# Kernel tuning notes

Measured on AMD Instinct MI355X. Metric: run time of the kernel, lower is better.

The kernel has to match this reference:

```python
import jax, jax.numpy as jnp
import numpy as np

B, S, C, OUT = 8, 2048, 1024, 1024

def setup_inputs() -> dict:
    key = jax.random.key(0)
    ks = jax.random.split(key, 10)
    s = C ** -0.5
    return {
        "input": jax.random.normal(ks[0], (B, S, C), jnp.float32),
        "memory": jax.random.normal(ks[1], (B, S, C), jnp.float32),
        "Wq": jax.random.normal(ks[2], (C, C), jnp.float32) * s,
        "bq": jnp.zeros((C,), jnp.float32),
        "Wk": jax.random.normal(ks[3], (C, C), jnp.float32) * s,
        "bk": jnp.zeros((C,), jnp.float32),
        "Wv": jax.random.normal(ks[4], (C, C), jnp.float32) * s,
        "bv": jnp.zeros((C,), jnp.float32),
        "Wo": jax.random.normal(ks[5], (OUT, C), jnp.float32) * s,
        "bo": jnp.zeros((OUT,), jnp.float32),
    }

def reference(input, memory, Wq, bq, Wk, bk, Wv, bv, Wo, bo):
    depth_scale = input.shape[2] ** -0.5
    q = (input @ Wq.T + bq) * depth_scale          # [B, Sq, C]
    k = memory @ Wk.T + bk                          # [B, Sk, C]
    v = memory @ Wv.T + bv                          # [B, Sk, C]
    logit = jnp.einsum('bqc,bkc->bqk', q, k)        # [B, Sq, Sk]
    attn = jax.nn.softmax(logit, axis=-1)
    sel = jnp.einsum('bqk,bkc->bqc', attn, v)       # [B, Sq, C]
    return sel @ Wo.T + bo                          # [B, Sq, OUT]
```

## Files before the change

### kernel.cpp

```cpp
#include <hip/hip_runtime.h>
#include <hip/hip_bf16.h>


typedef __attribute__((ext_vector_type(8))) short short8;
typedef __attribute__((ext_vector_type(4))) float f32x4;

static __device__ __forceinline__ unsigned short f2bf(float f) {
  union { float f; unsigned u; } x; x.f = f;
  unsigned r = x.u + 0x7FFFu + ((x.u >> 16) & 1u);
  return (unsigned short)(r >> 16);
}

static __device__ __forceinline__ long long brickoff(int r_, int k_, int Kd) {
  return (long long)(r_ >> 7) * ((long long)128 * Kd) +
         (long long)(k_ >> 5) * 4096 +
         (r_ & 127) * 32 +
         (((((k_ >> 3) & 3) ^ ((r_ >> 1) & 3))) << 3) +
         (k_ & 7);
}

__global__ __launch_bounds__(256) void cvt_brick_kernel(
    const float* __restrict__ s0, const float* __restrict__ s1,
    unsigned short* __restrict__ o0, unsigned short* __restrict__ o1,
    long long ngran) {
  const float* src = blockIdx.y ? s1 : s0;
  unsigned short* dst = blockIdx.y ? o1 : o0;
  long long gid = (long long)blockIdx.x * 256 + threadIdx.x;
  const long long stride = (long long)gridDim.x * 256;
  for (; gid < ngran; gid += stride) {
    const int tile = (int)(gid >> 14);
    const int g2 = (int)(gid & 16383);
    const int ks = g2 >> 9;
    const int rp = g2 & 511;
    const int r = rp >> 2;
    const int p = rp & 3;
    const int g = p ^ ((r >> 1) & 3);
    const float* sp = src + (long long)(tile * 128 + r) * 1024 + ks * 32 + g * 8;
    float4 u0 = ((const float4*)sp)[0];
    float4 u1 = ((const float4*)sp)[1];
    short8 pk;
    pk[0] = (short)f2bf(u0.x); pk[1] = (short)f2bf(u0.y);
    pk[2] = (short)f2bf(u0.z); pk[3] = (short)f2bf(u0.w);
    pk[4] = (short)f2bf(u1.x); pk[5] = (short)f2bf(u1.y);
    pk[6] = (short)f2bf(u1.z); pk[7] = (short)f2bf(u1.w);
    *(short8*)&dst[gid * 8] = pk;
  }
}

__global__ __launch_bounds__(256) void wcvt_brick_kernel(
    const float* __restrict__ w0, const float* __restrict__ w1,
    const float* __restrict__ w2, const float* __restrict__ w3,
    unsigned short* __restrict__ o0, unsigned short* __restrict__ o1,
    unsigned short* __restrict__ o2, unsigned short* __restrict__ o3) {
  const float* src; unsigned short* dst;
  switch (blockIdx.y) {
    case 0: src = w0; dst = o0; break;
    case 1: src = w1; dst = o1; break;
    case 2: src = w2; dst = o2; break;
    default: src = w3; dst = o3; break;
  }
  const int gid = blockIdx.x * 256 + threadIdx.x;
  const int tile = gid >> 14;
  const int g2 = gid & 16383;
  const int ks = g2 >> 9;
  const int rp = g2 & 511;
  const int r = rp >> 2;
  const int p = rp & 3;
  const int g = p ^ ((r >> 1) & 3);
  const float* sp = src + (long long)(tile * 128 + r) * 1024 + ks * 32 + g * 8;
  float4 u0 = ((const float4*)sp)[0];
  float4 u1 = ((const float4*)sp)[1];
  short8 pk;
  pk[0] = (short)f2bf(u0.x); pk[1] = (short)f2bf(u0.y);
  pk[2] = (short)f2bf(u0.z); pk[3] = (short)f2bf(u0.w);
  pk[4] = (short)f2bf(u1.x); pk[5] = (short)f2bf(u1.y);
  pk[6] = (short)f2bf(u1.z); pk[7] = (short)f2bf(u1.w);
  *(short8*)&dst[(long long)gid * 8] = pk;
}

#define EPI_BF16 0
#define EPI_BF16_TRANS 1
#define EPI_EXP 2
#define EPI_PV 3
#define EPI_F32 4

template <int EPI, bool HAS_BIAS>
__global__ __launch_bounds__(256, 3) void gemm_kernel(
    const unsigned short* __restrict__ A, const unsigned short* __restrict__ B,
    const float* __restrict__ bias, void* __restrict__ Dv,
    int NT, int ldaK, int ldbK, int ldd,
    long long sA, long long sBflat, int sBslice, int kOffB,
    long long sD, float scale) {
  int i = blockIdx.x + gridDim.x * (blockIdx.y + gridDim.y * blockIdx.z);
  const int nwg = gridDim.x * gridDim.y * gridDim.z;
  int v = (i & 7) * (nwg >> 3) + (i >> 3);
  const int by = v % gridDim.y;
  int u = v / gridDim.y;
  const int bx = u % gridDim.x;
  const int bz = u / gridDim.x;

  const int bm = bx * 128;
  const int bn = by * 128;
  const int tid = threadIdx.x;
  const int lane = tid & 63;
  const int wid = tid >> 6;
  const int wr = (wid >> 1) * 64;
  const int wc = (wid & 1) * 64;
  const int fr = lane & 15;
  const int hi = lane >> 4;
  const int laneoff = fr * 32 + ((hi ^ ((fr >> 1) & 3)) << 3);

  f32x4 acc[4][4];
#pragma unroll
  for (int m = 0; m < 4; ++m)
#pragma unroll
    for (int n = 0; n < 4; ++n) acc[m][n] = (f32x4){0.f, 0.f, 0.f, 0.f};

  f32x4 asum[4];
  short8 ones;
#pragma unroll
  for (int m = 0; m < 4; ++m) asum[m] = (f32x4){0.f, 0.f, 0.f, 0.f};
#pragma unroll
  for (int j = 0; j < 8; ++j) ones[j] = (short)0x3F80;

  const unsigned short* Ap = A + bz * sA + (long long)(bm >> 7) * 128 * ldaK +
                             wr * 32 + laneoff;
  const unsigned short* Bp = B + bz * sBflat + (long long)(bn >> 7) * 128 * ldbK +
                             (long long)(kOffB + bz * sBslice) * 4096 +
                             wc * 32 + laneoff;

  short8 a0[4], b0[4], a1[4], b1[4];
  auto LDA = [&](short8 (&d)[4], int t) {
    const unsigned short* p = Ap + (long long)t * 4096;
#pragma unroll
    for (int m = 0; m < 4; ++m) d[m] = *(const short8*)(p + m * 512);
  };
  auto LDB = [&](short8 (&d)[4], int t) {
    const unsigned short* p = Bp + (long long)t * 4096;
#pragma unroll
    for (int n = 0; n < 4; ++n) d[n] = *(const short8*)(p + n * 512);
  };
  auto FMA = [&](short8 (&a)[4], short8 (&b)[4]) {
#pragma unroll
    for (int m = 0; m < 4; ++m)
#pragma unroll
      for (int n = 0; n < 4; ++n)
        acc[m][n] = __builtin_amdgcn_mfma_f32_16x16x32_bf16(a[m], b[n],
                                                            acc[m][n], 0, 0, 0);
    if (EPI == EPI_PV) {
#pragma unroll
      for (int m = 0; m < 4; ++m)
        asum[m] = __builtin_amdgcn_mfma_f32_16x16x32_bf16(a[m], ones,
                                                          asum[m], 0, 0, 0);
    }
  };

  LDA(a0, 0); LDB(b0, 0);
  LDA(a1, 1); LDB(b1, 1);
  for (int t = 0; t < NT - 2; t += 2) {
    FMA(a0, b0);
    LDA(a0, t + 2); LDB(b0, t + 2);
    FMA(a1, b1);
    LDA(a1, t + 3); LDB(b1, t + 3);
  }
  FMA(a0, b0);
  FMA(a1, b1);

  const int cr = hi * 4;
  const int cc = fr;
#pragma unroll
  for (int m = 0; m < 4; ++m) {
    const int row0 = bm + wr + m * 16 + cr;
#pragma unroll
    for (int n = 0; n < 4; ++n) {
      const int col = bn + wc + n * 16 + cc;
      const float bv = HAS_BIAS ? bias[col] : 0.f;
      if (EPI == EPI_F32) {
        float* D = (float*)Dv + bz * sD;
#pragma unroll
        for (int j = 0; j < 4; ++j)
          D[(long long)(row0 + j) * ldd + col] = acc[m][n][j] + bv;
      } else if (EPI == EPI_BF16) {
        unsigned short* D = (unsigned short*)Dv + bz * sD;
#pragma unroll
        for (int j = 0; j < 4; ++j)
          D[brickoff(row0 + j, col, ldd)] = f2bf((acc[m][n][j] + bv) * scale);
      } else if (EPI == EPI_BF16_TRANS) {
        unsigned short* D = (unsigned short*)Dv + bz * sD;
#pragma unroll
        for (int j = 0; j < 4; ++j)
          D[brickoff(col, row0 + j, ldd)] = f2bf((acc[m][n][j] + bv) * scale);
      } else if (EPI == EPI_EXP) {
        unsigned short* D = (unsigned short*)Dv + bz * sD;
#pragma unroll
        for (int j = 0; j < 4; ++j)
          D[brickoff(row0 + j, col, ldd)] = f2bf(__expf(acc[m][n][j]));
      } else {
        unsigned short* D = (unsigned short*)Dv + bz * sD;
#pragma unroll
        for (int j = 0; j < 4; ++j) {
          const float li = 1.f / asum[m][j];
          D[brickoff(row0 + j, col, ldd)] = f2bf(acc[m][n][j] * li);
        }
      }
    }
  }
}

extern "C" void kernel_launch(void* const* d_in, const int* in_sizes, int n_in,
                              void* d_out, int out_size, void* d_ws, size_t ws_size,
                              hipStream_t stream) {
  (void)in_sizes; (void)n_in; (void)out_size;
  const float* input  = (const float*)d_in[0];
  const float* memory = (const float*)d_in[1];
  const float* Wq = (const float*)d_in[2];
  const float* bq = (const float*)d_in[3];
  const float* Wk = (const float*)d_in[4];
  const float* bk = (const float*)d_in[5];
  const float* Wv = (const float*)d_in[6];
  const float* bv = (const float*)d_in[7];
  const float* Wo = (const float*)d_in[8];
  const float* bo = (const float*)d_in[9];
  float* out = (float*)d_out;

  const int S = 2048, C = 1024;
  const int CB = 4;
  const long long BS = 16384;
  const long long N_IN = BS * C;
  const long long N_W  = (long long)C * C;

  char* p = (char*)d_ws;
  auto alloc = [&](size_t bytes) {
    char* r = p;
    p += (bytes + 255) & ~(size_t)255;
    return r;
  };
  unsigned short* wqb  = (unsigned short*)alloc(N_W * 2);
  unsigned short* wkb  = (unsigned short*)alloc(N_W * 2);
  unsigned short* wvb  = (unsigned short*)alloc(N_W * 2);
  unsigned short* wob  = (unsigned short*)alloc(N_W * 2);
  unsigned short* Qb   = (unsigned short*)alloc(N_IN * 2);
  unsigned short* Kb   = (unsigned short*)alloc(N_IN * 2);
  unsigned short* Xb   = (unsigned short*)alloc(N_IN * 2);
  if ((size_t)(p - (char*)d_ws) > ws_size) return;

  unsigned short* Vt  = (unsigned short*)d_out;
  unsigned short* inb = (unsigned short*)d_out + N_IN;
  unsigned short* memb = Xb;
  unsigned short* Pt   = Xb;

  wcvt_brick_kernel<<<dim3(512, 4, 1), 256, 0, stream>>>(Wq, Wk, Wv, Wo,
                                                         wqb, wkb, wvb, wob);
  cvt_brick_kernel<<<dim3(2048, 2, 1), 256, 0, stream>>>(memory, input, memb, inb,
                                                         N_IN / 8);

  const float depth_scale = 0.03125f;

  gemm_kernel<EPI_BF16, true><<<dim3(128, 8, 1), 256, 0, stream>>>(
      memb, wkb, bk, Kb, 32, C, C, C, 0, 0, 0, 0, 0, 1.0f);
  gemm_kernel<EPI_BF16_TRANS, true><<<dim3(128, 8, 1), 256, 0, stream>>>(
      memb, wvb, bv, Vt, 32, C, C, (int)BS, 0, 0, 0, 0, 0, 1.0f);
  gemm_kernel<EPI_BF16, true><<<dim3(128, 8, 1), 256, 0, stream>>>(
      inb, wqb, bq, Qb, 32, C, C, C, 0, 0, 0, 0, 0, depth_scale);

  for (int c = 0; c < 8 / CB; ++c) {
    const long long qoff = (long long)c * CB * S * C;
    gemm_kernel<EPI_EXP, false><<<dim3(16, 16, CB), 256, 0, stream>>>(
        Qb + qoff, Kb + qoff, nullptr, Pt,
        32, C, C, S, (long long)S * C, (long long)S * C, 0, 0,
        (long long)S * S, 1.0f);
    gemm_kernel<EPI_PV, false><<<dim3(16, 8, CB), 256, 0, stream>>>(
        Pt, Vt, nullptr, Qb + qoff,
        64, S, (int)BS, C, (long long)S * S, 0, 64, c * CB * 64,
        (long long)S * C, 1.0f);
  }

  gemm_kernel<EPI_F32, true><<<dim3(128, 8, 1), 256, 0, stream>>>(
      Qb, wob, bo, out, 32, C, C, C, 0, 0, 0, 0, 0, 1.0f);
}
```

Measured before the change: 396.0 us.

## Template GEMM tile shape to 128x256 and restructure activation bf16 conversion

The GEMM kernel becomes templated on per-wave fragment counts, so most GEMMs use a 128x256 block tile (4x8 fragments per wave), with occupancy lowered to 2 waves per SIMD for the larger tiles. This halves the grid in N and raises operand reuse per loaded A fragment, cutting global/L2 load traffic per MFMA. The activation conversion kernel now has each thread read a contiguous 32-float row segment and write four swizzled 8-element granules, instead of one granule per thread in a grid-stride loop. In exchange, the larger tiles raise register pressure and leave fewer workgroups to fill the CUs.

```diff
diff --git a/kernel.cpp b/kernel.cpp
--- a/kernel.cpp
+++ b/kernel.cpp
@@ -21,29 +21,30 @@
 
 __global__ __launch_bounds__(256) void cvt_brick_kernel(
     const float* __restrict__ s0, const float* __restrict__ s1,
-    unsigned short* __restrict__ o0, unsigned short* __restrict__ o1,
-    long long ngran) {
+    unsigned short* __restrict__ o0, unsigned short* __restrict__ o1) {
   const float* src = blockIdx.y ? s1 : s0;
   unsigned short* dst = blockIdx.y ? o1 : o0;
-  long long gid = (long long)blockIdx.x * 256 + threadIdx.x;
-  const long long stride = (long long)gridDim.x * 256;
-  for (; gid < ngran; gid += stride) {
-    const int tile = (int)(gid >> 14);
-    const int g2 = (int)(gid & 16383);
-    const int ks = g2 >> 9;
-    const int rp = g2 & 511;
-    const int r = rp >> 2;
-    const int p = rp & 3;
-    const int g = p ^ ((r >> 1) & 3);
-    const float* sp = src + (long long)(tile * 128 + r) * 1024 + ks * 32 + g * 8;
-    float4 u0 = ((const float4*)sp)[0];
-    float4 u1 = ((const float4*)sp)[1];
+  const int gid = blockIdx.x * 256 + threadIdx.x;
+  const int wv = gid >> 6;
+  const int lane = gid & 63;
+  const int tile = wv >> 6;
+  const int r = (wv & 63) * 2 + (lane & 1);
+  const int ks = lane >> 1;
+  const float* sp = src + (long long)(tile * 128 + r) * 1024 + ks * 32;
+  float4 u[8];
+#pragma unroll
+  for (int i = 0; i < 8; ++i) u[i] = ((const float4*)sp)[i];
+  const int x = (r >> 1) & 3;
+  unsigned short* dp = dst + (long long)tile * 131072 + ks * 4096 + r * 32;
+#pragma unroll
+  for (int p = 0; p < 4; ++p) {
+    const int g = p ^ x;
     short8 pk;
-    pk[0] = (short)f2bf(u0.x); pk[1] = (short)f2bf(u0.y);
-    pk[2] = (short)f2bf(u0.z); pk[3] = (short)f2bf(u0.w);
-    pk[4] = (short)f2bf(u1.x); pk[5] = (short)f2bf(u1.y);
-    pk[6] = (short)f2bf(u1.z); pk[7] = (short)f2bf(u1.w);
-    *(short8*)&dst[gid * 8] = pk;
+    pk[0] = (short)f2bf(u[2*g].x);   pk[1] = (short)f2bf(u[2*g].y);
+    pk[2] = (short)f2bf(u[2*g].z);   pk[3] = (short)f2bf(u[2*g].w);
+    pk[4] = (short)f2bf(u[2*g+1].x); pk[5] = (short)f2bf(u[2*g+1].y);
+    pk[6] = (short)f2bf(u[2*g+1].z); pk[7] = (short)f2bf(u[2*g+1].w);
+    *(short8*)(dp + p * 8) = pk;
   }
 }
 
@@ -84,13 +85,16 @@
 #define EPI_PV 3
 #define EPI_F32 4
 
-template <int EPI, bool HAS_BIAS>
-__global__ __launch_bounds__(256, 3) void gemm_kernel(
+template <int MFR, int NFR, int EPI, bool HAS_BIAS>
+__global__ __launch_bounds__(256, (MFR * NFR >= 32) ? 2 : 3) void gemm_kernel(
     const unsigned short* __restrict__ A, const unsigned short* __restrict__ B,
     const float* __restrict__ bias, void* __restrict__ Dv,
     int NT, int ldaK, int ldbK, int ldd,
     long long sA, long long sBflat, int sBslice, int kOffB,
     long long sD, float scale) {
+  constexpr int BM = MFR * 32;
+  constexpr int BN = NFR * 32;
+
   int i = blockIdx.x + gridDim.x * (blockIdx.y + gridDim.y * blockIdx.z);
   const int nwg = gridDim.x * gridDim.y * gridDim.z;
   int v = (i & 7) * (nwg >> 3) + (i >> 3);
@@ -99,57 +103,57 @@
   const int bx = u % gridDim.x;
   const int bz = u / gridDim.x;
 
-  const int bm = bx * 128;
-  const int bn = by * 128;
+  const int bm = bx * BM;
+  const int bn = by * BN;
   const int tid = threadIdx.x;
   const int lane = tid & 63;
   const int wid = tid >> 6;
-  const int wr = (wid >> 1) * 64;
-  const int wc = (wid & 1) * 64;
+  const int wr = (wid >> 1) * (MFR * 16);
+  const int wc = (wid & 1) * (NFR * 16);
   const int fr = lane & 15;
   const int hi = lane >> 4;
   const int laneoff = fr * 32 + ((hi ^ ((fr >> 1) & 3)) << 3);
 
-  f32x4 acc[4][4];
-#pragma unroll
-  for (int m = 0; m < 4; ++m)
-#pragma unroll
-    for (int n = 0; n < 4; ++n) acc[m][n] = (f32x4){0.f, 0.f, 0.f, 0.f};
-
-  f32x4 asum[4];
+  f32x4 acc[MFR][NFR];
+#pragma unroll
+  for (int m = 0; m < MFR; ++m)
+#pragma unroll
+    for (int n = 0; n < NFR; ++n) acc[m][n] = (f32x4){0.f, 0.f, 0.f, 0.f};
+
+  f32x4 asum[MFR];
   short8 ones;
 #pragma unroll
-  for (int m = 0; m < 4; ++m) asum[m] = (f32x4){0.f, 0.f, 0.f, 0.f};
+  for (int m = 0; m < MFR; ++m) asum[m] = (f32x4){0.f, 0.f, 0.f, 0.f};
 #pragma unroll
   for (int j = 0; j < 8; ++j) ones[j] = (short)0x3F80;
 
-  const unsigned short* Ap = A + bz * sA + (long long)(bm >> 7) * 128 * ldaK +
-                             wr * 32 + laneoff;
-  const unsigned short* Bp = B + bz * sBflat + (long long)(bn >> 7) * 128 * ldbK +
-                             (long long)(kOffB + bz * sBslice) * 4096 +
-                             wc * 32 + laneoff;
-
-  short8 a0[4], b0[4], a1[4], b1[4];
-  auto LDA = [&](short8 (&d)[4], int t) {
+  const unsigned short* Ap = A + bz * sA +
+      (long long)((bm + wr) >> 7) * 128 * ldaK + (wr & 127) * 32 + laneoff;
+  const unsigned short* Bp = B + bz * sBflat +
+      (long long)((bn + wc) >> 7) * 128 * ldbK +
+      (long long)(kOffB + bz * sBslice) * 4096 + (wc & 127) * 32 + laneoff;
+
+  short8 a0[MFR], b0[NFR], a1[MFR], b1[NFR];
+  auto LDA = [&](short8 (&d)[MFR], int t) {
     const unsigned short* p = Ap + (long long)t * 4096;
 #pragma unroll
-    for (int m = 0; m < 4; ++m) d[m] = *(const short8*)(p + m * 512);
-  };
-  auto LDB = [&](short8 (&d)[4], int t) {
+    for (int m = 0; m < MFR; ++m) d[m] = *(const short8*)(p + m * 512);
+  };
+  auto LDB = [&](short8 (&d)[NFR], int t) {
     const unsigned short* p = Bp + (long long)t * 4096;
 #pragma unroll
-    for (int n = 0; n < 4; ++n) d[n] = *(const short8*)(p + n * 512);
-  };
-  auto FMA = [&](short8 (&a)[4], short8 (&b)[4]) {
-#pragma unroll
-    for (int m = 0; m < 4; ++m)
-#pragma unroll
-      for (int n = 0; n < 4; ++n)
+    for (int n = 0; n < NFR; ++n) d[n] = *(const short8*)(p + n * 512);
+  };
+  auto FMA = [&](short8 (&a)[MFR], short8 (&b)[NFR]) {
+#pragma unroll
+    for (int m = 0; m < MFR; ++m)
+#pragma unroll
+      for (int n = 0; n < NFR; ++n)
         acc[m][n] = __builtin_amdgcn_mfma_f32_16x16x32_bf16(a[m], b[n],
                                                             acc[m][n], 0, 0, 0);
     if (EPI == EPI_PV) {
 #pragma unroll
-      for (int m = 0; m < 4; ++m)
+      for (int m = 0; m < MFR; ++m)
         asum[m] = __builtin_amdgcn_mfma_f32_16x16x32_bf16(a[m], ones,
                                                           asum[m], 0, 0, 0);
     }
@@ -169,10 +173,10 @@
   const int cr = hi * 4;
   const int cc = fr;
 #pragma unroll
-  for (int m = 0; m < 4; ++m) {
+  for (int m = 0; m < MFR; ++m) {
     const int row0 = bm + wr + m * 16 + cr;
 #pragma unroll
-    for (int n = 0; n < 4; ++n) {
+    for (int n = 0; n < NFR; ++n) {
       const int col = bn + wc + n * 16 + cc;
       const float bv = HAS_BIAS ? bias[col] : 0.f;
       if (EPI == EPI_F32) {
@@ -251,30 +255,29 @@
 
   wcvt_brick_kernel<<<dim3(512, 4, 1), 256, 0, stream>>>(Wq, Wk, Wv, Wo,
                                                          wqb, wkb, wvb, wob);
-  cvt_brick_kernel<<<dim3(2048, 2, 1), 256, 0, stream>>>(memory, input, memb, inb,
-                                                         N_IN / 8);
+  cvt_brick_kernel<<<dim3(2048, 2, 1), 256, 0, stream>>>(memory, input, memb, inb);
 
   const float depth_scale = 0.03125f;
 
-  gemm_kernel<EPI_BF16, true><<<dim3(128, 8, 1), 256, 0, stream>>>(
+  gemm_kernel<4, 8, EPI_BF16, true><<<dim3(128, 4, 1), 256, 0, stream>>>(
       memb, wkb, bk, Kb, 32, C, C, C, 0, 0, 0, 0, 0, 1.0f);
-  gemm_kernel<EPI_BF16_TRANS, true><<<dim3(128, 8, 1), 256, 0, stream>>>(
+  gemm_kernel<4, 8, EPI_BF16_TRANS, true><<<dim3(128, 4, 1), 256, 0, stream>>>(
       memb, wvb, bv, Vt, 32, C, C, (int)BS, 0, 0, 0, 0, 0, 1.0f);
-  gemm_kernel<EPI_BF16, true><<<dim3(128, 8, 1), 256, 0, stream>>>(
+  gemm_kernel<4, 8, EPI_BF16, true><<<dim3(128, 4, 1), 256, 0, stream>>>(
       inb, wqb, bq, Qb, 32, C, C, C, 0, 0, 0, 0, 0, depth_scale);
 
   for (int c = 0; c < 8 / CB; ++c) {
     const long long qoff = (long long)c * CB * S * C;
-    gemm_kernel<EPI_EXP, false><<<dim3(16, 16, CB), 256, 0, stream>>>(
+    gemm_kernel<4, 8, EPI_EXP, false><<<dim3(16, 8, CB), 256, 0, stream>>>(
         Qb + qoff, Kb + qoff, nullptr, Pt,
         32, C, C, S, (long long)S * C, (long long)S * C, 0, 0,
         (long long)S * S, 1.0f);
-    gemm_kernel<EPI_PV, false><<<dim3(16, 8, CB), 256, 0, stream>>>(
+    gemm_kernel<4, 4, EPI_PV, false><<<dim3(16, 8, CB), 256, 0, stream>>>(
         Pt, Vt, nullptr, Qb + qoff,
         64, S, (int)BS, C, (long long)S * S, 0, 64, c * CB * 64,
         (long long)S * C, 1.0f);
   }
 
-  gemm_kernel<EPI_F32, true><<<dim3(128, 8, 1), 256, 0, stream>>>(
+  gemm_kernel<4, 8, EPI_F32, true><<<dim3(128, 4, 1), 256, 0, stream>>>(
       Qb, wob, bo, out, 32, C, C, C, 0, 0, 0, 0, 0, 1.0f);
 }
```

Result: slower. 422.2 us (+6.6%).
